# Kernel tuning notes

Measured on AMD Instinct MI355X. Metric: run time of the kernel, lower is better.

The kernel has to match this reference:

```python
import jax, jax.numpy as jnp
import numpy as np

N_NODES = 50000
SHIFT = float(np.log(2.0))

def shifted_softplus(x):
    return jax.nn.softplus(x) - SHIFT

def setup_inputs() -> dict:
    key = jax.random.key(0)
    ks = jax.random.split(key, 5)
    N, E, F, H = N_NODES, 600000, 128, 128
    v = jax.random.normal(ks[0], (N, H), dtype=jnp.float32)
    e = jax.random.normal(ks[1], (E, F), dtype=jnp.float32)
    edge_index = jax.random.randint(ks[2], (2, E), 0, N, dtype=jnp.int64)
    # Xavier-uniform linear weights, zero bias (as in reset_parameters)
    lim1 = np.sqrt(6.0 / (F + H))
    w1 = jax.random.uniform(ks[3], (F, H), minval=-lim1, maxval=lim1, dtype=jnp.float32)
    b1 = jnp.zeros((H,), dtype=jnp.float32)
    lim2 = np.sqrt(6.0 / (H + H))
    w2 = jax.random.uniform(ks[4], (H, H), minval=-lim2, maxval=lim2, dtype=jnp.float32)
    b2 = jnp.zeros((H,), dtype=jnp.float32)
    return {"v": v, "e": e, "edge_index": edge_index, "w1": w1, "b1": b1, "w2": w2, "b2": b2}

def reference(v, e, edge_index, w1, b1, w2, b2):
    i = edge_index[1]  # target node per edge
    # scatter-sum edge messages into nodes: [E,F] -> [N,F]
    agg = jax.ops.segment_sum(e, i, num_segments=v.shape[0])
    out = shifted_softplus(agg @ w1 + b1)
    out = out @ w2 + b2
    return v + out
```

## Files before the change

### kernel.cpp

```cpp
#include <hip/hip_runtime.h>
#include <math.h>

#define HF 128
#define WPAD 136

typedef short bfrag __attribute__((ext_vector_type(8)));
typedef float facc  __attribute__((ext_vector_type(4)));
typedef float f4v   __attribute__((ext_vector_type(4)));

__device__ __forceinline__ unsigned short f2bf(float x) {
    unsigned int u = __float_as_uint(x);
    unsigned int r = (u + 0x7FFFu + ((u >> 16) & 1u)) >> 16;
    return (unsigned short)r;
}

__device__ __forceinline__ float ssp(float x) {
    const float SHIFT = 0.69314718055994531f;
    return (x > 0.f) ? (x + log1pf(expf(-x)) - SHIFT)
                     : (log1pf(expf(x)) - SHIFT);
}

__global__ void hist_kernel(const int* __restrict__ tgt, int* __restrict__ counts, int E) {
    int eid = blockIdx.x * blockDim.x + threadIdx.x;
    if (eid < E) atomicAdd(&counts[tgt[eid]], 1);
}

__global__ __launch_bounds__(1024) void scan1_kernel(const int* __restrict__ counts,
                                                     int* __restrict__ offsets,
                                                     int* __restrict__ bsum, int N) {
    __shared__ int ws[16];
    int t = threadIdx.x;
    int i = blockIdx.x * 1024 + t;
    int lane = t & 63, wv = t >> 6;
    int val = (i < N) ? counts[i] : 0;
    int x = val;
    #pragma unroll
    for (int d = 1; d < 64; d <<= 1) {
        int y = __shfl_up(x, d, 64);
        if (lane >= d) x += y;
    }
    if (lane == 63) ws[wv] = x;
    __syncthreads();
    if (wv == 0) {
        int s = (lane < 16) ? ws[lane] : 0;
        #pragma unroll
        for (int d = 1; d < 16; d <<= 1) {
            int y = __shfl_up(s, d, 64);
            if (lane >= d) s += y;
        }
        if (lane < 16) ws[lane] = s;
    }
    __syncthreads();
    int pre = ((wv > 0) ? ws[wv - 1] : 0) + (x - val);
    if (i < N) offsets[i] = pre;
    if (t == 0) bsum[blockIdx.x] = ws[15];
}

__global__ __launch_bounds__(1024) void scan23_kernel(int* __restrict__ offsets,
                                                      const int* __restrict__ bsum,
                                                      int N, int E, int nb) {
    __shared__ int pre_s;
    int t = threadIdx.x;
    if (t < 64) {
        int v = (t < nb && t < (int)blockIdx.x) ? bsum[t] : 0;
        #pragma unroll
        for (int d = 32; d > 0; d >>= 1) v += __shfl_down(v, d, 64);
        if (t == 0) pre_s = v;
    }
    __syncthreads();
    int i = blockIdx.x * 1024 + t;
    if (i < N) offsets[i] += pre_s;
    if (blockIdx.x == 0 && t == 0) offsets[N] = E;
}

__global__ void fill_kernel(const int* __restrict__ tgt, const int* __restrict__ offsets,
                            int* __restrict__ counts, int* __restrict__ edge_list, int E) {
    int eid = blockIdx.x * blockDim.x + threadIdx.x;
    if (eid >= E) return;
    int t = tgt[eid];
    int pos = atomicSub(&counts[t], 1) - 1;
    edge_list[offsets[t] + pos] = eid;
}

__global__ __launch_bounds__(256) void gather_kernel(const float* __restrict__ e,
                                                     const int* __restrict__ edge_list,
                                                     const int* __restrict__ offsets,
                                                     unsigned short* __restrict__ aggb, int N) {
    int wid = (blockIdx.x * blockDim.x + threadIdx.x) >> 6;
    if (wid >= N) return;
    int lane  = threadIdx.x & 63;
    int half  = lane >> 5;
    int chunk = lane & 31;
    int beg = offsets[wid], end = offsets[wid + 1];
    f4v acc0 = {0.f, 0.f, 0.f, 0.f};
    f4v acc1 = {0.f, 0.f, 0.f, 0.f};
    int j = beg;
    for (; j + 4 <= end; j += 4) {
        int ea = edge_list[j + half];
        int eb = edge_list[j + 2 + half];
        f4v ra = __builtin_nontemporal_load((const f4v*)(e + (size_t)ea * HF) + chunk);
        f4v rb = __builtin_nontemporal_load((const f4v*)(e + (size_t)eb * HF) + chunk);
        acc0 += ra;
        acc1 += rb;
    }
    for (; j < end; j += 2) {
        int jj = j + half;
        if (jj < end) {
            int ec = edge_list[jj];
            f4v rc = __builtin_nontemporal_load((const f4v*)(e + (size_t)ec * HF) + chunk);
            acc0 += rc;
        }
    }
    acc0 += acc1;
    acc0.x += __shfl_down(acc0.x, 32, 64);
    acc0.y += __shfl_down(acc0.y, 32, 64);
    acc0.z += __shfl_down(acc0.z, 32, 64);
    acc0.w += __shfl_down(acc0.w, 32, 64);
    if (lane < 32) {
        ushort4 o;
        o.x = f2bf(acc0.x); o.y = f2bf(acc0.y); o.z = f2bf(acc0.z); o.w = f2bf(acc0.w);
        ((ushort4*)(aggb + (size_t)wid * HF))[chunk] = o;
    }
}

__global__ __launch_bounds__(512) void mlp_mfma_kernel(
        const unsigned short* __restrict__ aggb,
        const float* __restrict__ v,
        const float* __restrict__ w1, const float* __restrict__ b1,
        const float* __restrict__ w2, const float* __restrict__ b2,
        float* __restrict__ out, int N, int ngroups) {
    __shared__ unsigned short wt1[HF * WPAD];
    __shared__ unsigned short wt2[HF * WPAD];
    __shared__ unsigned short atile[HF * WPAD];

    int tid = threadIdx.x;
    for (int idx = tid; idx < HF * HF; idx += 512) {
        int k = idx >> 7, n = idx & 127;
        wt1[n * WPAD + k] = f2bf(w1[idx]);
        wt2[n * WPAD + k] = f2bf(w2[idx]);
    }

    int w = tid >> 6, lane = tid & 63;
    int wr = (w & 3) * 32;
    int wchalf = (w >> 2) * 64;
    int lr = lane & 15;
    int kg = lane >> 4;
    float bias1[4], bias2[4];
    #pragma unroll
    for (int nt = 0; nt < 4; ++nt) {
        int col = wchalf + nt * 16 + lr;
        bias1[nt] = b1[col];
        bias2[nt] = b2[col];
    }

    for (int g = blockIdx.x; g < ngroups; g += gridDim.x) {
        int base = g * HF;
        __syncthreads();

        for (int idx = tid; idx < HF * 16; idx += 512) {
            int r = idx >> 4, c = idx & 15;
            int row = base + r;
            bfrag val = {0,0,0,0,0,0,0,0};
            if (row < N) val = *(const bfrag*)(aggb + (size_t)row * HF + c * 8);
            *(bfrag*)(atile + r * WPAD + c * 8) = val;
        }
        __syncthreads();

        facc acc[2][4];
        #pragma unroll
        for (int m = 0; m < 2; ++m)
            #pragma unroll
            for (int nt = 0; nt < 4; ++nt)
                acc[m][nt] = (facc){0.f, 0.f, 0.f, 0.f};
        #pragma unroll
        for (int ks = 0; ks < 4; ++ks) {
            int k0 = ks * 32 + kg * 8;
            bfrag a0 = *(const bfrag*)(atile + (wr + lr) * WPAD + k0);
            bfrag a1 = *(const bfrag*)(atile + (wr + 16 + lr) * WPAD + k0);
            #pragma unroll
            for (int nt = 0; nt < 4; ++nt) {
                bfrag b = *(const bfrag*)(wt1 + (wchalf + nt * 16 + lr) * WPAD + k0);
                acc[0][nt] = __builtin_amdgcn_mfma_f32_16x16x32_bf16(a0, b, acc[0][nt], 0, 0, 0);
                acc[1][nt] = __builtin_amdgcn_mfma_f32_16x16x32_bf16(a1, b, acc[1][nt], 0, 0, 0);
            }
        }
        __syncthreads();

        #pragma unroll
        for (int m = 0; m < 2; ++m) {
            int rbase = wr + m * 16 + kg * 4;
            #pragma unroll
            for (int nt = 0; nt < 4; ++nt) {
                int col = wchalf + nt * 16 + lr;
                #pragma unroll
                for (int i = 0; i < 4; ++i) {
                    float h = ssp(acc[m][nt][i] + bias1[nt]);
                    atile[(rbase + i) * WPAD + col] = f2bf(h);
                }
            }
        }
        __syncthreads();

        facc acc2[2][4];
        #pragma unroll
        for (int m = 0; m < 2; ++m)
            #pragma unroll
            for (int nt = 0; nt < 4; ++nt)
                acc2[m][nt] = (facc){0.f, 0.f, 0.f, 0.f};
        #pragma unroll
        for (int ks = 0; ks < 4; ++ks) {
            int k0 = ks * 32 + kg * 8;
            bfrag a0 = *(const bfrag*)(atile + (wr + lr) * WPAD + k0);
            bfrag a1 = *(const bfrag*)(atile + (wr + 16 + lr) * WPAD + k0);
            #pragma unroll
            for (int nt = 0; nt < 4; ++nt) {
                bfrag b = *(const bfrag*)(wt2 + (wchalf + nt * 16 + lr) * WPAD + k0);
                acc2[0][nt] = __builtin_amdgcn_mfma_f32_16x16x32_bf16(a0, b, acc2[0][nt], 0, 0, 0);
                acc2[1][nt] = __builtin_amdgcn_mfma_f32_16x16x32_bf16(a1, b, acc2[1][nt], 0, 0, 0);
            }
        }

        #pragma unroll
        for (int m = 0; m < 2; ++m) {
            #pragma unroll
            for (int i = 0; i < 4; ++i) {
                int row = base + wr + m * 16 + kg * 4 + i;
                if (row < N) {
                    #pragma unroll
                    for (int nt = 0; nt < 4; ++nt) {
                        int col = wchalf + nt * 16 + lr;
                        out[(size_t)row * HF + col] = acc2[m][nt][i] + bias2[nt] + v[(size_t)row * HF + col];
                    }
                }
            }
        }
    }
}

__global__ void scatter_add_kernel(const float* __restrict__ e,
                                   const int* __restrict__ tgt,
                                   float* __restrict__ agg, int E) {
    int t = blockIdx.x * blockDim.x + threadIdx.x;
    int eid = t >> 5;
    if (eid >= E) return;
    int c = t & 31;
    int dst = tgt[eid];
    float4 val = *reinterpret_cast<const float4*>(e + (size_t)eid * HF + c * 4);
    float* p = agg + (size_t)dst * HF + c * 4;
    unsafeAtomicAdd(p + 0, val.x);
    unsafeAtomicAdd(p + 1, val.y);
    unsafeAtomicAdd(p + 2, val.z);
    unsafeAtomicAdd(p + 3, val.w);
}

__device__ __forceinline__ void fma4(float4& acc, float a, const float4& w) {
    acc.x = fmaf(a, w.x, acc.x);
    acc.y = fmaf(a, w.y, acc.y);
    acc.z = fmaf(a, w.z, acc.z);
    acc.w = fmaf(a, w.w, acc.w);
}

__global__ __launch_bounds__(512) void mlp_kernel(
        float* __restrict__ data, const float* __restrict__ v,
        const float* __restrict__ w1, const float* __restrict__ b1,
        const float* __restrict__ w2, const float* __restrict__ b2, int N) {
    __shared__ float w1s[HF * HF];
    __shared__ float w2s[HF * HF];
    __shared__ float tile[32][HF];
    int tid = threadIdx.x;
    float4* w1sv = (float4*)w1s; float4* w2sv = (float4*)w2s;
    for (int i = tid; i < HF * HF / 4; i += 512) {
        w1sv[i] = ((const float4*)w1)[i];
        w2sv[i] = ((const float4*)w2)[i];
    }
    int nl = tid >> 5, fblk = tid & 31;
    float4 bb1 = ((const float4*)b1)[fblk];
    float4 bb2 = ((const float4*)b2)[fblk];
    float4* tilev = (float4*)tile;
    int ngroups = (N + 31) / 32;
    for (int g = blockIdx.x; g < ngroups; g += gridDim.x) {
        int base = g * 32;
        __syncthreads();
        for (int i = tid; i < 32 * (HF / 4); i += 512) {
            int node = base + (i >> 5);
            float4 val = make_float4(0.f, 0.f, 0.f, 0.f);
            if (node < N) val = ((const float4*)data)[(size_t)node * (HF / 4) + (i & 31)];
            tilev[i] = val;
        }
        __syncthreads();
        float4 a0 = bb1, a1 = bb1;
        #pragma unroll 8
        for (int k = 0; k < HF; ++k) {
            float x0 = tile[nl][k], x1 = tile[nl + 16][k];
            float4 w = w1sv[k * 32 + fblk];
            fma4(a0, x0, w); fma4(a1, x1, w);
        }
        a0.x = ssp(a0.x); a0.y = ssp(a0.y); a0.z = ssp(a0.z); a0.w = ssp(a0.w);
        a1.x = ssp(a1.x); a1.y = ssp(a1.y); a1.z = ssp(a1.z); a1.w = ssp(a1.w);
        __syncthreads();
        tilev[nl * 32 + fblk] = a0;
        tilev[(nl + 16) * 32 + fblk] = a1;
        __syncthreads();
        float4 c0 = bb2, c1 = bb2;
        #pragma unroll 8
        for (int k = 0; k < HF; ++k) {
            float x0 = tile[nl][k], x1 = tile[nl + 16][k];
            float4 w = w2sv[k * 32 + fblk];
            fma4(c0, x0, w); fma4(c1, x1, w);
        }
        int n0 = base + nl, n1 = base + nl + 16;
        if (n0 < N) {
            float4 vv = ((const float4*)v)[(size_t)n0 * 32 + fblk];
            c0.x += vv.x; c0.y += vv.y; c0.z += vv.z; c0.w += vv.w;
            ((float4*)data)[(size_t)n0 * 32 + fblk] = c0;
        }
        if (n1 < N) {
            float4 vv = ((const float4*)v)[(size_t)n1 * 32 + fblk];
            c1.x += vv.x; c1.y += vv.y; c1.z += vv.z; c1.w += vv.w;
            ((float4*)data)[(size_t)n1 * 32 + fblk] = c1;
        }
    }
}

extern "C" void kernel_launch(void* const* d_in, const int* in_sizes, int n_in,
                              void* d_out, int out_size, void* d_ws, size_t ws_size,
                              hipStream_t stream) {
    const float* v  = (const float*)d_in[0];
    const float* e  = (const float*)d_in[1];
    const int*   ei = (const int*)d_in[2];
    const float* w1 = (const float*)d_in[3];
    const float* b1 = (const float*)d_in[4];
    const float* w2 = (const float*)d_in[5];
    const float* b2 = (const float*)d_in[6];
    float* out = (float*)d_out;

    int N = in_sizes[0] / HF;
    int E = in_sizes[2] / 2;
    const int* tgt = ei + E;

    size_t ints = (size_t)N + (N + 1) + 64 + E;
    size_t needed = ints * 4 + 16 + (size_t)N * HF * 2;
    if (ws_size >= needed) {
        int* counts    = (int*)d_ws;
        int* offsets   = counts + N;
        int* bsum      = offsets + N + 1;
        int* edge_list = bsum + 64;
        uintptr_t p = (uintptr_t)(edge_list + E);
        p = (p + 15) & ~(uintptr_t)15;
        unsigned short* aggb = (unsigned short*)p;

        hipMemsetAsync(counts, 0, (size_t)N * sizeof(int), stream);

        int eb = (E + 255) / 256;
        int nb = (N + 1023) / 1024;
        hist_kernel<<<eb, 256, 0, stream>>>(tgt, counts, E);
        scan1_kernel<<<nb, 1024, 0, stream>>>(counts, offsets, bsum, N);
        scan23_kernel<<<nb, 1024, 0, stream>>>(offsets, bsum, N, E, nb);
        fill_kernel<<<eb, 256, 0, stream>>>(tgt, offsets, counts, edge_list, E);

        gather_kernel<<<(N + 3) / 4, 256, 0, stream>>>(e, edge_list, offsets, aggb, N);

        int ngroups = (N + HF - 1) / HF;
        mlp_mfma_kernel<<<256, 512, 0, stream>>>(aggb, v, w1, b1, w2, b2, out, N, ngroups);
    } else {
        hipMemsetAsync(out, 0, (size_t)N * HF * sizeof(float), stream);
        long long total_t = (long long)E * 32;
        scatter_add_kernel<<<(int)((total_t + 255) / 256), 256, 0, stream>>>(e, tgt, out, E);
        mlp_kernel<<<512, 512, 0, stream>>>(out, v, w1, b1, w2, b2, N);
    }
}
```

Baseline: 210.3 us.

## Scatter edges into sorted bf16 buffer, then sum contiguous rows per node

Replaces the edge-index fill plus indirect fp32 gather with a kernel that reads each edge row once, converts it to bf16, and writes it into its CSR-sorted slot. A second kernel then sums each node's contiguous bf16 rows with simple strided loads. The aim is sequential reads in the reduction and half the bytes read there. In exchange it adds a full E×128 bf16 write plus a reread, needs a much larger workspace, and rounds the inputs to bf16 before summation, which costs accuracy.

```diff
diff --git a/kernel.cpp b/kernel.cpp
--- a/kernel.cpp
+++ b/kernel.cpp
@@ -13,6 +13,8 @@
     unsigned int r = (u + 0x7FFFu + ((u >> 16) & 1u)) >> 16;
     return (unsigned short)r;
 }
+__device__ __forceinline__ float bflo(unsigned int u) { return __uint_as_float(u << 16); }
+__device__ __forceinline__ float bfhi(unsigned int u) { return __uint_as_float(u & 0xffff0000u); }
 
 __device__ __forceinline__ float ssp(float x) {
     const float SHIFT = 0.69314718055994531f;
@@ -73,54 +75,81 @@
     if (blockIdx.x == 0 && t == 0) offsets[N] = E;
 }
 
-__global__ void fill_kernel(const int* __restrict__ tgt, const int* __restrict__ offsets,
-                            int* __restrict__ counts, int* __restrict__ edge_list, int E) {
-    int eid = blockIdx.x * blockDim.x + threadIdx.x;
+__global__ __launch_bounds__(256) void scatter_convert_kernel(
+        const float* __restrict__ e, const int* __restrict__ tgt,
+        const int* __restrict__ offsets, int* __restrict__ counts,
+        unsigned short* __restrict__ es, int E) {
+    int wave = (blockIdx.x * blockDim.x + threadIdx.x) >> 6;
+    int lane = threadIdx.x & 63;
+    int half = lane >> 5, l32 = lane & 31;
+    int eid = wave * 2 + half;
     if (eid >= E) return;
     int t = tgt[eid];
-    int pos = atomicSub(&counts[t], 1) - 1;
-    edge_list[offsets[t] + pos] = eid;
-}
-
-__global__ __launch_bounds__(256) void gather_kernel(const float* __restrict__ e,
-                                                     const int* __restrict__ edge_list,
-                                                     const int* __restrict__ offsets,
-                                                     unsigned short* __restrict__ aggb, int N) {
-    int wid = (blockIdx.x * blockDim.x + threadIdx.x) >> 6;
-    if (wid >= N) return;
-    int lane  = threadIdx.x & 63;
-    int half  = lane >> 5;
-    int chunk = lane & 31;
-    int beg = offsets[wid], end = offsets[wid + 1];
-    f4v acc0 = {0.f, 0.f, 0.f, 0.f};
-    f4v acc1 = {0.f, 0.f, 0.f, 0.f};
+    int pos = 0;
+    if (l32 == 0) pos = atomicSub(&counts[t], 1) - 1;
+    pos = __shfl(pos, 0, 32);
+    int slot = offsets[t] + pos;
+    f4v r = __builtin_nontemporal_load((const f4v*)(e + (size_t)eid * HF) + l32);
+    ushort4 o;
+    o.x = f2bf(r.x); o.y = f2bf(r.y); o.z = f2bf(r.z); o.w = f2bf(r.w);
+    ((ushort4*)(es + (size_t)slot * HF))[l32] = o;
+}
+
+__global__ __launch_bounds__(256) void gather_seq_kernel(
+        const unsigned short* __restrict__ es, const int* __restrict__ offsets,
+        unsigned short* __restrict__ aggb, int N) {
+    int node = (blockIdx.x * blockDim.x + threadIdx.x) >> 6;
+    if (node >= N) return;
+    int lane = threadIdx.x & 63;
+    const unsigned int* rp = (const unsigned int*)es;
+    int beg = offsets[node], end = offsets[node + 1];
+    float s0 = 0.f, s1 = 0.f, t0 = 0.f, t1 = 0.f;
+    float u0 = 0.f, u1 = 0.f, v0 = 0.f, v1 = 0.f;
     int j = beg;
-    for (; j + 4 <= end; j += 4) {
-        int ea = edge_list[j + half];
-        int eb = edge_list[j + 2 + half];
-        f4v ra = __builtin_nontemporal_load((const f4v*)(e + (size_t)ea * HF) + chunk);
-        f4v rb = __builtin_nontemporal_load((const f4v*)(e + (size_t)eb * HF) + chunk);
-        acc0 += ra;
-        acc1 += rb;
-    }
-    for (; j < end; j += 2) {
-        int jj = j + half;
-        if (jj < end) {
-            int ec = edge_list[jj];
-            f4v rc = __builtin_nontemporal_load((const f4v*)(e + (size_t)ec * HF) + chunk);
-            acc0 += rc;
-        }
-    }
-    acc0 += acc1;
-    acc0.x += __shfl_down(acc0.x, 32, 64);
-    acc0.y += __shfl_down(acc0.y, 32, 64);
-    acc0.z += __shfl_down(acc0.z, 32, 64);
-    acc0.w += __shfl_down(acc0.w, 32, 64);
-    if (lane < 32) {
-        ushort4 o;
-        o.x = f2bf(acc0.x); o.y = f2bf(acc0.y); o.z = f2bf(acc0.z); o.w = f2bf(acc0.w);
-        ((ushort4*)(aggb + (size_t)wid * HF))[chunk] = o;
-    }
+    for (; j + 8 <= end; j += 8) {
+        unsigned int a0 = rp[(size_t)(j + 0) * 64 + lane];
+        unsigned int a1 = rp[(size_t)(j + 1) * 64 + lane];
+        unsigned int a2 = rp[(size_t)(j + 2) * 64 + lane];
+        unsigned int a3 = rp[(size_t)(j + 3) * 64 + lane];
+        unsigned int a4 = rp[(size_t)(j + 4) * 64 + lane];
+        unsigned int a5 = rp[(size_t)(j + 5) * 64 + lane];
+        unsigned int a6 = rp[(size_t)(j + 6) * 64 + lane];
+        unsigned int a7 = rp[(size_t)(j + 7) * 64 + lane];
+        s0 += bflo(a0); s1 += bfhi(a0);
+        t0 += bflo(a1); t1 += bfhi(a1);
+        u0 += bflo(a2); u1 += bfhi(a2);
+        v0 += bflo(a3); v1 += bfhi(a3);
+        s0 += bflo(a4); s1 += bfhi(a4);
+        t0 += bflo(a5); t1 += bfhi(a5);
+        u0 += bflo(a6); u1 += bfhi(a6);
+        v0 += bflo(a7); v1 += bfhi(a7);
+    }
+    if (j + 4 <= end) {
+        unsigned int a0 = rp[(size_t)(j + 0) * 64 + lane];
+        unsigned int a1 = rp[(size_t)(j + 1) * 64 + lane];
+        unsigned int a2 = rp[(size_t)(j + 2) * 64 + lane];
+        unsigned int a3 = rp[(size_t)(j + 3) * 64 + lane];
+        s0 += bflo(a0); s1 += bfhi(a0);
+        t0 += bflo(a1); t1 += bfhi(a1);
+        u0 += bflo(a2); u1 += bfhi(a2);
+        v0 += bflo(a3); v1 += bfhi(a3);
+        j += 4;
+    }
+    if (j + 2 <= end) {
+        unsigned int a0 = rp[(size_t)(j + 0) * 64 + lane];
+        unsigned int a1 = rp[(size_t)(j + 1) * 64 + lane];
+        s0 += bflo(a0); s1 += bfhi(a0);
+        t0 += bflo(a1); t1 += bfhi(a1);
+        j += 2;
+    }
+    if (j < end) {
+        unsigned int a0 = rp[(size_t)j * 64 + lane];
+        s0 += bflo(a0); s1 += bfhi(a0);
+    }
+    s0 += t0 + u0 + v0;
+    s1 += t1 + u1 + v1;
+    unsigned int out = ((unsigned int)f2bf(s1) << 16) | (unsigned int)f2bf(s0);
+    ((unsigned int*)aggb)[(size_t)node * 64 + lane] = out;
 }
 
 __global__ __launch_bounds__(512) void mlp_mfma_kernel(
@@ -338,16 +367,16 @@
     int E = in_sizes[2] / 2;
     const int* tgt = ei + E;
 
-    size_t ints = (size_t)N + (N + 1) + 64 + E;
-    size_t needed = ints * 4 + 16 + (size_t)N * HF * 2;
+    size_t ints = (size_t)N + (N + 1) + 64;
+    size_t needed = ints * 4 + 32 + (size_t)E * HF * 2 + (size_t)N * HF * 2;
     if (ws_size >= needed) {
-        int* counts    = (int*)d_ws;
-        int* offsets   = counts + N;
-        int* bsum      = offsets + N + 1;
-        int* edge_list = bsum + 64;
-        uintptr_t p = (uintptr_t)(edge_list + E);
+        int* counts  = (int*)d_ws;
+        int* offsets = counts + N;
+        int* bsum    = offsets + N + 1;
+        uintptr_t p = (uintptr_t)(bsum + 64);
         p = (p + 15) & ~(uintptr_t)15;
-        unsigned short* aggb = (unsigned short*)p;
+        unsigned short* es = (unsigned short*)p;
+        unsigned short* aggb = es + (size_t)E * HF;
 
         hipMemsetAsync(counts, 0, (size_t)N * sizeof(int), stream);
 
@@ -356,9 +385,11 @@
         hist_kernel<<<eb, 256, 0, stream>>>(tgt, counts, E);
         scan1_kernel<<<nb, 1024, 0, stream>>>(counts, offsets, bsum, N);
         scan23_kernel<<<nb, 1024, 0, stream>>>(offsets, bsum, N, E, nb);
-        fill_kernel<<<eb, 256, 0, stream>>>(tgt, offsets, counts, edge_list, E);
-
-        gather_kernel<<<(N + 3) / 4, 256, 0, stream>>>(e, edge_list, offsets, aggb, N);
+
+        int scb = (E + 7) / 8;
+        scatter_convert_kernel<<<scb, 256, 0, stream>>>(e, tgt, offsets, counts, es, E);
+
+        gather_seq_kernel<<<(N + 3) / 4, 256, 0, stream>>>(es, offsets, aggb, N);
 
         int ngroups = (N + HF - 1) / HF;
         mlp_mfma_kernel<<<256, 512, 0, stream>>>(aggb, v, w1, b1, w2, b2, out, N, ngroups);
```

Result: slower. 242.7 us (+15.4%).

## Pre-convert edges to bf16 and fuse gather into MLP kernel

Applied to the files above, without the earlier changes.

Adds a kernel that converts the whole edge feature tensor to packed bf16 while computing the target histogram. The per-node gather now runs inside the MLP kernel, one block per 128-node tile, writing sums straight into shared memory instead of an aggb buffer. W1 and W2 share one LDS buffer, loaded in turn. This is meant to halve the bytes of the random gather and drop the intermediate buffer. In exchange it adds a full extra read and write pass over e and rounds each edge to bf16 before summation. The workspace requirement also grows greatly.

```diff
diff --git a/kernel.cpp b/kernel.cpp
--- a/kernel.cpp
+++ b/kernel.cpp
@@ -13,6 +13,8 @@
     unsigned int r = (u + 0x7FFFu + ((u >> 16) & 1u)) >> 16;
     return (unsigned short)r;
 }
+__device__ __forceinline__ float bflo(unsigned int u) { return __uint_as_float(u << 16); }
+__device__ __forceinline__ float bfhi(unsigned int u) { return __uint_as_float(u & 0xffff0000u); }
 
 __device__ __forceinline__ float ssp(float x) {
     const float SHIFT = 0.69314718055994531f;
@@ -20,9 +22,21 @@
                      : (log1pf(expf(x)) - SHIFT);
 }
 
-__global__ void hist_kernel(const int* __restrict__ tgt, int* __restrict__ counts, int E) {
-    int eid = blockIdx.x * blockDim.x + threadIdx.x;
-    if (eid < E) atomicAdd(&counts[tgt[eid]], 1);
+__global__ __launch_bounds__(256) void conv_hist_kernel(
+        const float* __restrict__ e, const int* __restrict__ tgt,
+        int* __restrict__ counts, unsigned int* __restrict__ eb,
+        long long nq, int E) {
+    long long stride = (long long)gridDim.x * blockDim.x;
+    long long tid = (long long)blockIdx.x * blockDim.x + threadIdx.x;
+    for (long long i = tid; i < nq; i += stride) {
+        f4v r = __builtin_nontemporal_load(((const f4v*)e) + i);
+        uint2 o;
+        o.x = ((unsigned int)f2bf(r.y) << 16) | f2bf(r.x);
+        o.y = ((unsigned int)f2bf(r.w) << 16) | f2bf(r.z);
+        ((uint2*)eb)[i] = o;
+    }
+    for (long long i = tid; i < E; i += stride)
+        atomicAdd(&counts[tgt[i]], 1);
 }
 
 __global__ __launch_bounds__(1024) void scan1_kernel(const int* __restrict__ counts,
@@ -82,65 +96,67 @@
     edge_list[offsets[t] + pos] = eid;
 }
 
-__global__ __launch_bounds__(256) void gather_kernel(const float* __restrict__ e,
-                                                     const int* __restrict__ edge_list,
-                                                     const int* __restrict__ offsets,
-                                                     unsigned short* __restrict__ aggb, int N) {
-    int wid = (blockIdx.x * blockDim.x + threadIdx.x) >> 6;
-    if (wid >= N) return;
-    int lane  = threadIdx.x & 63;
-    int half  = lane >> 5;
-    int chunk = lane & 31;
-    int beg = offsets[wid], end = offsets[wid + 1];
-    f4v acc0 = {0.f, 0.f, 0.f, 0.f};
-    f4v acc1 = {0.f, 0.f, 0.f, 0.f};
-    int j = beg;
-    for (; j + 4 <= end; j += 4) {
-        int ea = edge_list[j + half];
-        int eb = edge_list[j + 2 + half];
-        f4v ra = __builtin_nontemporal_load((const f4v*)(e + (size_t)ea * HF) + chunk);
-        f4v rb = __builtin_nontemporal_load((const f4v*)(e + (size_t)eb * HF) + chunk);
-        acc0 += ra;
-        acc1 += rb;
-    }
-    for (; j < end; j += 2) {
-        int jj = j + half;
-        if (jj < end) {
-            int ec = edge_list[jj];
-            f4v rc = __builtin_nontemporal_load((const f4v*)(e + (size_t)ec * HF) + chunk);
-            acc0 += rc;
-        }
-    }
-    acc0 += acc1;
-    acc0.x += __shfl_down(acc0.x, 32, 64);
-    acc0.y += __shfl_down(acc0.y, 32, 64);
-    acc0.z += __shfl_down(acc0.z, 32, 64);
-    acc0.w += __shfl_down(acc0.w, 32, 64);
-    if (lane < 32) {
-        ushort4 o;
-        o.x = f2bf(acc0.x); o.y = f2bf(acc0.y); o.z = f2bf(acc0.z); o.w = f2bf(acc0.w);
-        ((ushort4*)(aggb + (size_t)wid * HF))[chunk] = o;
-    }
-}
-
-__global__ __launch_bounds__(512) void mlp_mfma_kernel(
-        const unsigned short* __restrict__ aggb,
+__global__ __launch_bounds__(512) void mlp_fused_kernel(
+        const unsigned int* __restrict__ eb,
+        const int* __restrict__ edge_list,
+        const int* __restrict__ offsets,
         const float* __restrict__ v,
         const float* __restrict__ w1, const float* __restrict__ b1,
         const float* __restrict__ w2, const float* __restrict__ b2,
-        float* __restrict__ out, int N, int ngroups) {
-    __shared__ unsigned short wt1[HF * WPAD];
-    __shared__ unsigned short wt2[HF * WPAD];
+        float* __restrict__ out, int N) {
+    __shared__ unsigned short wt[HF * WPAD];
     __shared__ unsigned short atile[HF * WPAD];
 
     int tid = threadIdx.x;
+    int w = tid >> 6, lane = tid & 63;
+    int base = blockIdx.x * HF;
+
+    #pragma unroll 1
+    for (int i = 0; i < 16; ++i) {
+        int nl = w * 16 + i;
+        int node = base + nl;
+        float s0 = 0.f, s1 = 0.f, t0 = 0.f, t1 = 0.f;
+        float u0 = 0.f, u1 = 0.f, p0 = 0.f, p1 = 0.f;
+        if (node < N) {
+            int beg = offsets[node], end = offsets[node + 1];
+            int j = beg;
+            for (; j + 4 <= end; j += 4) {
+                int e0 = edge_list[j + 0];
+                int e1 = edge_list[j + 1];
+                int e2 = edge_list[j + 2];
+                int e3 = edge_list[j + 3];
+                unsigned int a0 = eb[(size_t)e0 * 64 + lane];
+                unsigned int a1 = eb[(size_t)e1 * 64 + lane];
+                unsigned int a2 = eb[(size_t)e2 * 64 + lane];
+                unsigned int a3 = eb[(size_t)e3 * 64 + lane];
+                s0 += bflo(a0); s1 += bfhi(a0);
+                t0 += bflo(a1); t1 += bfhi(a1);
+                u0 += bflo(a2); u1 += bfhi(a2);
+                p0 += bflo(a3); p1 += bfhi(a3);
+            }
+            if (j + 2 <= end) {
+                unsigned int a0 = eb[(size_t)edge_list[j + 0] * 64 + lane];
+                unsigned int a1 = eb[(size_t)edge_list[j + 1] * 64 + lane];
+                s0 += bflo(a0); s1 += bfhi(a0);
+                t0 += bflo(a1); t1 += bfhi(a1);
+                j += 2;
+            }
+            if (j < end) {
+                unsigned int a0 = eb[(size_t)edge_list[j] * 64 + lane];
+                s0 += bflo(a0); s1 += bfhi(a0);
+            }
+        }
+        s0 += t0 + u0 + p0;
+        s1 += t1 + u1 + p1;
+        unsigned int o = ((unsigned int)f2bf(s1) << 16) | f2bf(s0);
+        *(unsigned int*)(atile + nl * WPAD + lane * 2) = o;
+    }
+
     for (int idx = tid; idx < HF * HF; idx += 512) {
         int k = idx >> 7, n = idx & 127;
-        wt1[n * WPAD + k] = f2bf(w1[idx]);
-        wt2[n * WPAD + k] = f2bf(w2[idx]);
-    }
-
-    int w = tid >> 6, lane = tid & 63;
+        wt[n * WPAD + k] = f2bf(w1[idx]);
+    }
+
     int wr = (w & 3) * 32;
     int wchalf = (w >> 2) * 64;
     int lr = lane & 15;
@@ -153,84 +169,76 @@
         bias2[nt] = b2[col];
     }
 
-    for (int g = blockIdx.x; g < ngroups; g += gridDim.x) {
-        int base = g * HF;
-        __syncthreads();
-
-        for (int idx = tid; idx < HF * 16; idx += 512) {
-            int r = idx >> 4, c = idx & 15;
-            int row = base + r;
-            bfrag val = {0,0,0,0,0,0,0,0};
-            if (row < N) val = *(const bfrag*)(aggb + (size_t)row * HF + c * 8);
-            *(bfrag*)(atile + r * WPAD + c * 8) = val;
-        }
-        __syncthreads();
-
-        facc acc[2][4];
-        #pragma unroll
-        for (int m = 0; m < 2; ++m)
-            #pragma unroll
-            for (int nt = 0; nt < 4; ++nt)
-                acc[m][nt] = (facc){0.f, 0.f, 0.f, 0.f};
-        #pragma unroll
-        for (int ks = 0; ks < 4; ++ks) {
-            int k0 = ks * 32 + kg * 8;
-            bfrag a0 = *(const bfrag*)(atile + (wr + lr) * WPAD + k0);
-            bfrag a1 = *(const bfrag*)(atile + (wr + 16 + lr) * WPAD + k0);
-            #pragma unroll
-            for (int nt = 0; nt < 4; ++nt) {
-                bfrag b = *(const bfrag*)(wt1 + (wchalf + nt * 16 + lr) * WPAD + k0);
-                acc[0][nt] = __builtin_amdgcn_mfma_f32_16x16x32_bf16(a0, b, acc[0][nt], 0, 0, 0);
-                acc[1][nt] = __builtin_amdgcn_mfma_f32_16x16x32_bf16(a1, b, acc[1][nt], 0, 0, 0);
-            }
-        }
-        __syncthreads();
-
-        #pragma unroll
-        for (int m = 0; m < 2; ++m) {
-            int rbase = wr + m * 16 + kg * 4;
-            #pragma unroll
-            for (int nt = 0; nt < 4; ++nt) {
-                int col = wchalf + nt * 16 + lr;
-                #pragma unroll
-                for (int i = 0; i < 4; ++i) {
-                    float h = ssp(acc[m][nt][i] + bias1[nt]);
-                    atile[(rbase + i) * WPAD + col] = f2bf(h);
-                }
-            }
-        }
-        __syncthreads();
-
-        facc acc2[2][4];
-        #pragma unroll
-        for (int m = 0; m < 2; ++m)
-            #pragma unroll
-            for (int nt = 0; nt < 4; ++nt)
-                acc2[m][nt] = (facc){0.f, 0.f, 0.f, 0.f};
-        #pragma unroll
-        for (int ks = 0; ks < 4; ++ks) {
-            int k0 = ks * 32 + kg * 8;
-            bfrag a0 = *(const bfrag*)(atile + (wr + lr) * WPAD + k0);
-            bfrag a1 = *(const bfrag*)(atile + (wr + 16 + lr) * WPAD + k0);
-            #pragma unroll
-            for (int nt = 0; nt < 4; ++nt) {
-                bfrag b = *(const bfrag*)(wt2 + (wchalf + nt * 16 + lr) * WPAD + k0);
-                acc2[0][nt] = __builtin_amdgcn_mfma_f32_16x16x32_bf16(a0, b, acc2[0][nt], 0, 0, 0);
-                acc2[1][nt] = __builtin_amdgcn_mfma_f32_16x16x32_bf16(a1, b, acc2[1][nt], 0, 0, 0);
-            }
-        }
-
-        #pragma unroll
-        for (int m = 0; m < 2; ++m) {
+    __syncthreads();
+
+    facc acc[2][4];
+    #pragma unroll
+    for (int m = 0; m < 2; ++m)
+        #pragma unroll
+        for (int nt = 0; nt < 4; ++nt)
+            acc[m][nt] = (facc){0.f, 0.f, 0.f, 0.f};
+    #pragma unroll
+    for (int ks = 0; ks < 4; ++ks) {
+        int k0 = ks * 32 + kg * 8;
+        bfrag a0 = *(const bfrag*)(atile + (wr + lr) * WPAD + k0);
+        bfrag a1 = *(const bfrag*)(atile + (wr + 16 + lr) * WPAD + k0);
+        #pragma unroll
+        for (int nt = 0; nt < 4; ++nt) {
+            bfrag b = *(const bfrag*)(wt + (wchalf + nt * 16 + lr) * WPAD + k0);
+            acc[0][nt] = __builtin_amdgcn_mfma_f32_16x16x32_bf16(a0, b, acc[0][nt], 0, 0, 0);
+            acc[1][nt] = __builtin_amdgcn_mfma_f32_16x16x32_bf16(a1, b, acc[1][nt], 0, 0, 0);
+        }
+    }
+    __syncthreads();
+
+    for (int idx = tid; idx < HF * HF; idx += 512) {
+        int k = idx >> 7, n = idx & 127;
+        wt[n * WPAD + k] = f2bf(w2[idx]);
+    }
+    #pragma unroll
+    for (int m = 0; m < 2; ++m) {
+        int rbase = wr + m * 16 + kg * 4;
+        #pragma unroll
+        for (int nt = 0; nt < 4; ++nt) {
+            int col = wchalf + nt * 16 + lr;
             #pragma unroll
             for (int i = 0; i < 4; ++i) {
-                int row = base + wr + m * 16 + kg * 4 + i;
-                if (row < N) {
-                    #pragma unroll
-                    for (int nt = 0; nt < 4; ++nt) {
-                        int col = wchalf + nt * 16 + lr;
-                        out[(size_t)row * HF + col] = acc2[m][nt][i] + bias2[nt] + v[(size_t)row * HF + col];
-                    }
+                float h = ssp(acc[m][nt][i] + bias1[nt]);
+                atile[(rbase + i) * WPAD + col] = f2bf(h);
+            }
+        }
+    }
+    __syncthreads();
+
+    facc acc2[2][4];
+    #pragma unroll
+    for (int m = 0; m < 2; ++m)
+        #pragma unroll
+        for (int nt = 0; nt < 4; ++nt)
+            acc2[m][nt] = (facc){0.f, 0.f, 0.f, 0.f};
+    #pragma unroll
+    for (int ks = 0; ks < 4; ++ks) {
+        int k0 = ks * 32 + kg * 8;
+        bfrag a0 = *(const bfrag*)(atile + (wr + lr) * WPAD + k0);
+        bfrag a1 = *(const bfrag*)(atile + (wr + 16 + lr) * WPAD + k0);
+        #pragma unroll
+        for (int nt = 0; nt < 4; ++nt) {
+            bfrag b = *(const bfrag*)(wt + (wchalf + nt * 16 + lr) * WPAD + k0);
+            acc2[0][nt] = __builtin_amdgcn_mfma_f32_16x16x32_bf16(a0, b, acc2[0][nt], 0, 0, 0);
+            acc2[1][nt] = __builtin_amdgcn_mfma_f32_16x16x32_bf16(a1, b, acc2[1][nt], 0, 0, 0);
+        }
+    }
+
+    #pragma unroll
+    for (int m = 0; m < 2; ++m) {
+        #pragma unroll
+        for (int i = 0; i < 4; ++i) {
+            int row = base + wr + m * 16 + kg * 4 + i;
+            if (row < N) {
+                #pragma unroll
+                for (int nt = 0; nt < 4; ++nt) {
+                    int col = wchalf + nt * 16 + lr;
+                    out[(size_t)row * HF + col] = acc2[m][nt][i] + bias2[nt] + v[(size_t)row * HF + col];
                 }
             }
         }
@@ -339,7 +347,7 @@
     const int* tgt = ei + E;
 
     size_t ints = (size_t)N + (N + 1) + 64 + E;
-    size_t needed = ints * 4 + 16 + (size_t)N * HF * 2;
+    size_t needed = ints * 4 + 32 + (size_t)E * HF * 2;
     if (ws_size >= needed) {
         int* counts    = (int*)d_ws;
         int* offsets   = counts + N;
@@ -347,21 +355,21 @@
         int* edge_list = bsum + 64;
         uintptr_t p = (uintptr_t)(edge_list + E);
         p = (p + 15) & ~(uintptr_t)15;
-        unsigned short* aggb = (unsigned short*)p;
+        unsigned int* eb = (unsigned int*)p;
 
         hipMemsetAsync(counts, 0, (size_t)N * sizeof(int), stream);
 
-        int eb = (E + 255) / 256;
+        long long nq = (long long)E * 32;
+        conv_hist_kernel<<<2048, 256, 0, stream>>>(e, tgt, counts, eb, nq, E);
+
         int nb = (N + 1023) / 1024;
-        hist_kernel<<<eb, 256, 0, stream>>>(tgt, counts, E);
         scan1_kernel<<<nb, 1024, 0, stream>>>(counts, offsets, bsum, N);
         scan23_kernel<<<nb, 1024, 0, stream>>>(offsets, bsum, N, E, nb);
-        fill_kernel<<<eb, 256, 0, stream>>>(tgt, offsets, counts, edge_list, E);
-
-        gather_kernel<<<(N + 3) / 4, 256, 0, stream>>>(e, edge_list, offsets, aggb, N);
+        fill_kernel<<<(E + 255) / 256, 256, 0, stream>>>(tgt, offsets, counts, edge_list, E);
 
         int ngroups = (N + HF - 1) / HF;
-        mlp_mfma_kernel<<<256, 512, 0, stream>>>(aggb, v, w1, b1, w2, b2, out, N, ngroups);
+        mlp_fused_kernel<<<ngroups, 512, 0, stream>>>(eb, edge_list, offsets, v,
+                                                      w1, b1, w2, b2, out, N);
     } else {
         hipMemsetAsync(out, 0, (size_t)N * HF * sizeof(float), stream);
         long long total_t = (long long)E * 32;
```

Measured after the change: 249.9 us. 18.9% more time.

## Use half-wave per node in gather and one tile per MLP block

Applied to the files above, without the earlier changes.

The gather kernel now assigns 32 lanes per node instead of a full 64-lane wave, with four independent accumulators, so the cross-half shuffle reduction goes away and more loads are in flight per thread. The MLP kernel drops the persistent grid-stride loop and launches one block per 128-row tile. It keeps a single shared weight buffer that is reloaded with w2 after the first GEMM, which cuts LDS use and may allow higher occupancy. The cost is that every block now converts both weight matrices, where before those conversions were amortised across many tiles.

```diff
diff --git a/kernel.cpp b/kernel.cpp
--- a/kernel.cpp
+++ b/kernel.cpp
@@ -86,41 +86,40 @@
                                                      const int* __restrict__ edge_list,
                                                      const int* __restrict__ offsets,
                                                      unsigned short* __restrict__ aggb, int N) {
-    int wid = (blockIdx.x * blockDim.x + threadIdx.x) >> 6;
-    if (wid >= N) return;
-    int lane  = threadIdx.x & 63;
-    int half  = lane >> 5;
-    int chunk = lane & 31;
-    int beg = offsets[wid], end = offsets[wid + 1];
-    f4v acc0 = {0.f, 0.f, 0.f, 0.f};
-    f4v acc1 = {0.f, 0.f, 0.f, 0.f};
+    int node = (blockIdx.x * blockDim.x + threadIdx.x) >> 5;
+    if (node >= N) return;
+    int chunk = threadIdx.x & 31;
+    int beg = offsets[node], end = offsets[node + 1];
+    f4v a0 = {0.f, 0.f, 0.f, 0.f};
+    f4v a1 = {0.f, 0.f, 0.f, 0.f};
+    f4v a2 = {0.f, 0.f, 0.f, 0.f};
+    f4v a3 = {0.f, 0.f, 0.f, 0.f};
     int j = beg;
     for (; j + 4 <= end; j += 4) {
-        int ea = edge_list[j + half];
-        int eb = edge_list[j + 2 + half];
-        f4v ra = __builtin_nontemporal_load((const f4v*)(e + (size_t)ea * HF) + chunk);
-        f4v rb = __builtin_nontemporal_load((const f4v*)(e + (size_t)eb * HF) + chunk);
-        acc0 += ra;
-        acc1 += rb;
-    }
-    for (; j < end; j += 2) {
-        int jj = j + half;
-        if (jj < end) {
-            int ec = edge_list[jj];
-            f4v rc = __builtin_nontemporal_load((const f4v*)(e + (size_t)ec * HF) + chunk);
-            acc0 += rc;
-        }
-    }
-    acc0 += acc1;
-    acc0.x += __shfl_down(acc0.x, 32, 64);
-    acc0.y += __shfl_down(acc0.y, 32, 64);
-    acc0.z += __shfl_down(acc0.z, 32, 64);
-    acc0.w += __shfl_down(acc0.w, 32, 64);
-    if (lane < 32) {
-        ushort4 o;
-        o.x = f2bf(acc0.x); o.y = f2bf(acc0.y); o.z = f2bf(acc0.z); o.w = f2bf(acc0.w);
-        ((ushort4*)(aggb + (size_t)wid * HF))[chunk] = o;
-    }
+        int e0 = edge_list[j + 0];
+        int e1 = edge_list[j + 1];
+        int e2 = edge_list[j + 2];
+        int e3 = edge_list[j + 3];
+        a0 += __builtin_nontemporal_load((const f4v*)(e + (size_t)e0 * HF) + chunk);
+        a1 += __builtin_nontemporal_load((const f4v*)(e + (size_t)e1 * HF) + chunk);
+        a2 += __builtin_nontemporal_load((const f4v*)(e + (size_t)e2 * HF) + chunk);
+        a3 += __builtin_nontemporal_load((const f4v*)(e + (size_t)e3 * HF) + chunk);
+    }
+    if (j + 2 <= end) {
+        int e0 = edge_list[j + 0];
+        int e1 = edge_list[j + 1];
+        a0 += __builtin_nontemporal_load((const f4v*)(e + (size_t)e0 * HF) + chunk);
+        a1 += __builtin_nontemporal_load((const f4v*)(e + (size_t)e1 * HF) + chunk);
+        j += 2;
+    }
+    if (j < end) {
+        int e0 = edge_list[j];
+        a2 += __builtin_nontemporal_load((const f4v*)(e + (size_t)e0 * HF) + chunk);
+    }
+    a0 += a1; a2 += a3; a0 += a2;
+    ushort4 o;
+    o.x = f2bf(a0.x); o.y = f2bf(a0.y); o.z = f2bf(a0.z); o.w = f2bf(a0.w);
+    ((ushort4*)(aggb + (size_t)node * HF))[chunk] = o;
 }
 
 __global__ __launch_bounds__(512) void mlp_mfma_kernel(
@@ -128,16 +127,23 @@
         const float* __restrict__ v,
         const float* __restrict__ w1, const float* __restrict__ b1,
         const float* __restrict__ w2, const float* __restrict__ b2,
-        float* __restrict__ out, int N, int ngroups) {
-    __shared__ unsigned short wt1[HF * WPAD];
-    __shared__ unsigned short wt2[HF * WPAD];
+        float* __restrict__ out, int N) {
+    __shared__ unsigned short wt[HF * WPAD];
     __shared__ unsigned short atile[HF * WPAD];
 
     int tid = threadIdx.x;
+    int base = blockIdx.x * HF;
+
+    for (int idx = tid; idx < HF * 16; idx += 512) {
+        int r = idx >> 4, c = idx & 15;
+        int row = base + r;
+        bfrag val = {0,0,0,0,0,0,0,0};
+        if (row < N) val = *(const bfrag*)(aggb + (size_t)row * HF + c * 8);
+        *(bfrag*)(atile + r * WPAD + c * 8) = val;
+    }
     for (int idx = tid; idx < HF * HF; idx += 512) {
         int k = idx >> 7, n = idx & 127;
-        wt1[n * WPAD + k] = f2bf(w1[idx]);
-        wt2[n * WPAD + k] = f2bf(w2[idx]);
+        wt[n * WPAD + k] = f2bf(w1[idx]);
     }
 
     int w = tid >> 6, lane = tid & 63;
@@ -152,85 +158,76 @@
         bias1[nt] = b1[col];
         bias2[nt] = b2[col];
     }
-
-    for (int g = blockIdx.x; g < ngroups; g += gridDim.x) {
-        int base = g * HF;
-        __syncthreads();
-
-        for (int idx = tid; idx < HF * 16; idx += 512) {
-            int r = idx >> 4, c = idx & 15;
-            int row = base + r;
-            bfrag val = {0,0,0,0,0,0,0,0};
-            if (row < N) val = *(const bfrag*)(aggb + (size_t)row * HF + c * 8);
-            *(bfrag*)(atile + r * WPAD + c * 8) = val;
-        }
-        __syncthreads();
-
-        facc acc[2][4];
-        #pragma unroll
-        for (int m = 0; m < 2; ++m)
-            #pragma unroll
-            for (int nt = 0; nt < 4; ++nt)
-                acc[m][nt] = (facc){0.f, 0.f, 0.f, 0.f};
-        #pragma unroll
-        for (int ks = 0; ks < 4; ++ks) {
-            int k0 = ks * 32 + kg * 8;
-            bfrag a0 = *(const bfrag*)(atile + (wr + lr) * WPAD + k0);
-            bfrag a1 = *(const bfrag*)(atile + (wr + 16 + lr) * WPAD + k0);
-            #pragma unroll
-            for (int nt = 0; nt < 4; ++nt) {
-                bfrag b = *(const bfrag*)(wt1 + (wchalf + nt * 16 + lr) * WPAD + k0);
-                acc[0][nt] = __builtin_amdgcn_mfma_f32_16x16x32_bf16(a0, b, acc[0][nt], 0, 0, 0);
-                acc[1][nt] = __builtin_amdgcn_mfma_f32_16x16x32_bf16(a1, b, acc[1][nt], 0, 0, 0);
-            }
-        }
-        __syncthreads();
-
-        #pragma unroll
-        for (int m = 0; m < 2; ++m) {
-            int rbase = wr + m * 16 + kg * 4;
-            #pragma unroll
-            for (int nt = 0; nt < 4; ++nt) {
-                int col = wchalf + nt * 16 + lr;
-                #pragma unroll
-                for (int i = 0; i < 4; ++i) {
-                    float h = ssp(acc[m][nt][i] + bias1[nt]);
-                    atile[(rbase + i) * WPAD + col] = f2bf(h);
-                }
-            }
-        }
-        __syncthreads();
-
-        facc acc2[2][4];
-        #pragma unroll
-        for (int m = 0; m < 2; ++m)
-            #pragma unroll
-            for (int nt = 0; nt < 4; ++nt)
-                acc2[m][nt] = (facc){0.f, 0.f, 0.f, 0.f};
-        #pragma unroll
-        for (int ks = 0; ks < 4; ++ks) {
-            int k0 = ks * 32 + kg * 8;
-            bfrag a0 = *(const bfrag*)(atile + (wr + lr) * WPAD + k0);
-            bfrag a1 = *(const bfrag*)(atile + (wr + 16 + lr) * WPAD + k0);
-            #pragma unroll
-            for (int nt = 0; nt < 4; ++nt) {
-                bfrag b = *(const bfrag*)(wt2 + (wchalf + nt * 16 + lr) * WPAD + k0);
-                acc2[0][nt] = __builtin_amdgcn_mfma_f32_16x16x32_bf16(a0, b, acc2[0][nt], 0, 0, 0);
-                acc2[1][nt] = __builtin_amdgcn_mfma_f32_16x16x32_bf16(a1, b, acc2[1][nt], 0, 0, 0);
-            }
-        }
-
-        #pragma unroll
-        for (int m = 0; m < 2; ++m) {
+    __syncthreads();
+
+    facc acc[2][4];
+    #pragma unroll
+    for (int m = 0; m < 2; ++m)
+        #pragma unroll
+        for (int nt = 0; nt < 4; ++nt)
+            acc[m][nt] = (facc){0.f, 0.f, 0.f, 0.f};
+    #pragma unroll
+    for (int ks = 0; ks < 4; ++ks) {
+        int k0 = ks * 32 + kg * 8;
+        bfrag a0 = *(const bfrag*)(atile + (wr + lr) * WPAD + k0);
+        bfrag a1 = *(const bfrag*)(atile + (wr + 16 + lr) * WPAD + k0);
+        #pragma unroll
+        for (int nt = 0; nt < 4; ++nt) {
+            bfrag b = *(const bfrag*)(wt + (wchalf + nt * 16 + lr) * WPAD + k0);
+            acc[0][nt] = __builtin_amdgcn_mfma_f32_16x16x32_bf16(a0, b, acc[0][nt], 0, 0, 0);
+            acc[1][nt] = __builtin_amdgcn_mfma_f32_16x16x32_bf16(a1, b, acc[1][nt], 0, 0, 0);
+        }
+    }
+    __syncthreads();
+
+    for (int idx = tid; idx < HF * HF; idx += 512) {
+        int k = idx >> 7, n = idx & 127;
+        wt[n * WPAD + k] = f2bf(w2[idx]);
+    }
+    #pragma unroll
+    for (int m = 0; m < 2; ++m) {
+        int rbase = wr + m * 16 + kg * 4;
+        #pragma unroll
+        for (int nt = 0; nt < 4; ++nt) {
+            int col = wchalf + nt * 16 + lr;
             #pragma unroll
             for (int i = 0; i < 4; ++i) {
-                int row = base + wr + m * 16 + kg * 4 + i;
-                if (row < N) {
-                    #pragma unroll
-                    for (int nt = 0; nt < 4; ++nt) {
-                        int col = wchalf + nt * 16 + lr;
-                        out[(size_t)row * HF + col] = acc2[m][nt][i] + bias2[nt] + v[(size_t)row * HF + col];
-                    }
+                float h = ssp(acc[m][nt][i] + bias1[nt]);
+                atile[(rbase + i) * WPAD + col] = f2bf(h);
+            }
+        }
+    }
+    __syncthreads();
+
+    facc acc2[2][4];
+    #pragma unroll
+    for (int m = 0; m < 2; ++m)
+        #pragma unroll
+        for (int nt = 0; nt < 4; ++nt)
+            acc2[m][nt] = (facc){0.f, 0.f, 0.f, 0.f};
+    #pragma unroll
+    for (int ks = 0; ks < 4; ++ks) {
+        int k0 = ks * 32 + kg * 8;
+        bfrag a0 = *(const bfrag*)(atile + (wr + lr) * WPAD + k0);
+        bfrag a1 = *(const bfrag*)(atile + (wr + 16 + lr) * WPAD + k0);
+        #pragma unroll
+        for (int nt = 0; nt < 4; ++nt) {
+            bfrag b = *(const bfrag*)(wt + (wchalf + nt * 16 + lr) * WPAD + k0);
+            acc2[0][nt] = __builtin_amdgcn_mfma_f32_16x16x32_bf16(a0, b, acc2[0][nt], 0, 0, 0);
+            acc2[1][nt] = __builtin_amdgcn_mfma_f32_16x16x32_bf16(a1, b, acc2[1][nt], 0, 0, 0);
+        }
+    }
+
+    #pragma unroll
+    for (int m = 0; m < 2; ++m) {
+        #pragma unroll
+        for (int i = 0; i < 4; ++i) {
+            int row = base + wr + m * 16 + kg * 4 + i;
+            if (row < N) {
+                #pragma unroll
+                for (int nt = 0; nt < 4; ++nt) {
+                    int col = wchalf + nt * 16 + lr;
+                    out[(size_t)row * HF + col] = acc2[m][nt][i] + bias2[nt] + v[(size_t)row * HF + col];
                 }
             }
         }
@@ -358,10 +355,10 @@
         scan23_kernel<<<nb, 1024, 0, stream>>>(offsets, bsum, N, E, nb);
         fill_kernel<<<eb, 256, 0, stream>>>(tgt, offsets, counts, edge_list, E);
 
-        gather_kernel<<<(N + 3) / 4, 256, 0, stream>>>(e, edge_list, offsets, aggb, N);
+        gather_kernel<<<(N + 7) / 8, 256, 0, stream>>>(e, edge_list, offsets, aggb, N);
 
         int ngroups = (N + HF - 1) / HF;
-        mlp_mfma_kernel<<<256, 512, 0, stream>>>(aggb, v, w1, b1, w2, b2, out, N, ngroups);
+        mlp_mfma_kernel<<<ngroups, 512, 0, stream>>>(aggb, v, w1, b1, w2, b2, out, N);
     } else {
         hipMemsetAsync(out, 0, (size_t)N * HF * sizeof(float), stream);
         long long total_t = (long long)E * 32;
```

Result: faster. 200.4 us (-4.7%).
